# Optimization experiments

Measured on AMD Instinct MI355X. Metric: run time of the kernel, lower is better.

Reference implementation:

```python
import jax, jax.numpy as jnp
import numpy as np

N_NODES = 50000   # number of graph nodes
N_EDGES = 800000  # avg degree 16
D = 128           # in_dim == all hdims -> residual active every layer
L = 3             # len(cfg['hdims'])


def setup_inputs() -> dict:
    key = jax.random.key(0)
    ks = jax.random.split(key, 8)
    scale = 1.0 / np.sqrt(D)
    x = jax.random.normal(ks[0], (N_NODES, D), dtype=jnp.float32)
    edge_index = jax.random.randint(ks[1], (2, N_EDGES), 0, N_NODES, dtype=jnp.int32)
    in_fc_w = jax.random.normal(ks[2], (D, D), dtype=jnp.float32) * scale
    in_fc_b = jnp.zeros((D,), dtype=jnp.float32)
    # GraphConv per layer: lin_rel (with bias) applied to aggregated neighbors,
    # lin_root (no bias) applied to self features. All layers are DxD -> stack.
    w_rel = jax.random.normal(ks[3], (L, D, D), dtype=jnp.float32) * scale
    b_rel = jnp.zeros((L, D), dtype=jnp.float32)
    w_root = jax.random.normal(ks[4], (L, D, D), dtype=jnp.float32) * scale
    return {"x": x, "edge_index": edge_index, "in_fc_w": in_fc_w,
            "in_fc_b": in_fc_b, "w_rel": w_rel, "b_rel": b_rel, "w_root": w_root}


def reference(x, edge_index, in_fc_w, in_fc_b, w_rel, b_rel, w_root):
    src, dst = edge_index[0], edge_index[1]
    h = x @ in_fc_w + in_fc_b                     # in_fc
    for l in range(L):                            # fixed small layer count
        # GraphConv, aggr='add': gather source feats, scatter-add to targets
        agg = jax.ops.segment_sum(h[src], dst, num_segments=N_NODES)  # [N, D]
        out = agg @ w_rel[l] + b_rel[l] + h @ w_root[l]
        out = jax.nn.relu(out)
        h = out + h                               # residual (dims match)
    return h
```

## Files before the change

### kernel.cpp

```cpp
#include <hip/hip_runtime.h>
#include <hip/hip_bf16.h>


constexpr int D = 128;
constexpr int NB_SHIFT = 7;
constexpr int BCAP = 2560;
constexpr int CHUNK = 2048;

typedef __attribute__((ext_vector_type(8))) short bf16x8;
typedef __attribute__((ext_vector_type(4))) float f32x4;
typedef __attribute__((ext_vector_type(4))) unsigned int u32x4;

__device__ inline unsigned short f2bf(float f) {
    unsigned int u = __builtin_bit_cast(unsigned int, f);
    u += 0x7FFFu + ((u >> 16) & 1u);
    return (unsigned short)(u >> 16);
}
__device__ inline float bf2f(unsigned short v) {
    return __builtin_bit_cast(float, (unsigned int)v << 16);
}
__device__ inline float bf2f_lo(unsigned int v) {
    return __builtin_bit_cast(float, v << 16);
}
__device__ inline float bf2f_hi(unsigned int v) {
    return __builtin_bit_cast(float, v & 0xFFFF0000u);
}

__global__ __launch_bounds__(256) void prep(
    const float* __restrict__ x, const float* __restrict__ fc_w,
    const float* __restrict__ w_rel, const float* __restrict__ w_root,
    unsigned short* __restrict__ xb, unsigned short* __restrict__ Wp,
    int* __restrict__ cursor, int n4, int NB)
{
    int blk = blockIdx.x;
    const int nconv = (n4 + 255) / 256;
    if (blk < nconv) {
        int i = blk * 256 + threadIdx.x;
        if (i < n4) {
            float4 v = ((const float4*)x)[i];
            ushort4 o;
            o.x = f2bf(v.x); o.y = f2bf(v.y); o.z = f2bf(v.z); o.w = f2bf(v.w);
            ((ushort4*)xb)[i] = o;
        }
        return;
    }
    blk -= nconv;
    if (blk < 56) {
        int idx = blk * 256 + threadIdx.x;
        int mat  = idx >> 11;
        int rem  = idx & 2047;
        int tn   = rem >> 8;
        int ks   = (rem >> 6) & 3;
        int lane = rem & 63;
        const float* w = (mat == 0) ? fc_w
                       : (mat <= 3) ? w_rel  + (size_t)(mat - 1) * D * D
                                    : w_root + (size_t)(mat - 4) * D * D;
        unsigned short* wp = Wp + (size_t)mat * D * D + (size_t)rem * 8;
        int kbase = ks * 32 + (lane >> 4) * 8;
        int col   = tn * 16 + (lane & 15);
        #pragma unroll
        for (int j = 0; j < 8; ++j)
            wp[j] = f2bf(w[(size_t)(kbase + j) * D + col]);
        return;
    }
    blk -= 56;
    int i = blk * 256 + threadIdx.x;
    if (i < NB) cursor[i] = 0;
}

__global__ __launch_bounds__(256) void gemm_mfma(
    const unsigned short* __restrict__ A1, const unsigned short* __restrict__ W1p,
    const float* __restrict__ bias, unsigned short* __restrict__ hb_out, int N)
{
    const int tid  = threadIdx.x;
    const int wave = tid >> 6;
    const int lane = tid & 63;
    const int row0 = blockIdx.x * 64 + wave * 16;
    const int mrow = lane & 15;
    const int kgrp = lane >> 4;

    f32x4 acc[8];
    #pragma unroll
    for (int t = 0; t < 8; ++t) acc[t] = (f32x4){0.f, 0.f, 0.f, 0.f};

    int arow = row0 + mrow; if (arow >= N) arow = N - 1;
    const size_t abase = (size_t)arow * D + kgrp * 8;

    #pragma unroll
    for (int ks = 0; ks < 4; ++ks) {
        bf16x8 a1 = *(const bf16x8*)(A1 + abase + ks * 32);
        #pragma unroll
        for (int tn = 0; tn < 8; ++tn) {
            bf16x8 b = *(const bf16x8*)(W1p + ((size_t)((tn * 4 + ks) * 64 + lane) * 8));
            acc[tn] = __builtin_amdgcn_mfma_f32_16x16x32_bf16(a1, b, acc[tn], 0, 0, 0);
        }
    }

    const int r0 = row0 + kgrp * 4;
    #pragma unroll
    for (int tn = 0; tn < 8; ++tn) {
        const int col = tn * 16 + mrow;
        const float bv = bias[col];
        #pragma unroll
        for (int reg = 0; reg < 4; ++reg) {
            int r = r0 + reg;
            if (r < N) hb_out[(size_t)r * D + col] = f2bf(acc[tn][reg] + bv);
        }
    }
}

__global__ __launch_bounds__(256) void layer_fused(
    const unsigned short* __restrict__ hb_in, const int* __restrict__ rs4,
    const unsigned short* __restrict__ sorted_src,
    const unsigned short* __restrict__ Wrel, const unsigned short* __restrict__ Wroot,
    const float* __restrict__ bias,
    unsigned short* hb_out, float* out_f32, int N)
{
    __shared__ unsigned short aggt[16][136];

    const int tid   = threadIdx.x;
    const int wave  = tid >> 6;
    const int lane  = tid & 63;
    const int node0 = blockIdx.x * 16;

    {
        const int g = lane >> 4;
        const int c = lane & 15;
        const int n = node0 + wave * 4 + g;

        float acc[8];
        #pragma unroll
        for (int q = 0; q < 8; ++q) acc[q] = 0.f;

        if (n < N) {
            const int b = rs4[n << 2];
            const int e = rs4[(n << 2) + 4];
            int j = b;
            for (; j + 8 <= e; j += 8) {
                int s0 = sorted_src[j];
                int s1 = sorted_src[j + 1];
                int s2 = sorted_src[j + 2];
                int s3 = sorted_src[j + 3];
                int s4 = sorted_src[j + 4];
                int s5 = sorted_src[j + 5];
                int s6 = sorted_src[j + 6];
                int s7 = sorted_src[j + 7];
                u32x4 v0 = *(const u32x4*)((const unsigned int*)(hb_in + (size_t)s0 * D) + c * 4);
                u32x4 v1 = *(const u32x4*)((const unsigned int*)(hb_in + (size_t)s1 * D) + c * 4);
                u32x4 v2 = *(const u32x4*)((const unsigned int*)(hb_in + (size_t)s2 * D) + c * 4);
                u32x4 v3 = *(const u32x4*)((const unsigned int*)(hb_in + (size_t)s3 * D) + c * 4);
                u32x4 v4 = *(const u32x4*)((const unsigned int*)(hb_in + (size_t)s4 * D) + c * 4);
                u32x4 v5 = *(const u32x4*)((const unsigned int*)(hb_in + (size_t)s5 * D) + c * 4);
                u32x4 v6 = *(const u32x4*)((const unsigned int*)(hb_in + (size_t)s6 * D) + c * 4);
                u32x4 v7 = *(const u32x4*)((const unsigned int*)(hb_in + (size_t)s7 * D) + c * 4);
                #pragma unroll
                for (int q = 0; q < 4; ++q) {
                    acc[2 * q]     += ((bf2f_lo(v0[q]) + bf2f_lo(v1[q])) + (bf2f_lo(v2[q]) + bf2f_lo(v3[q])))
                                    + ((bf2f_lo(v4[q]) + bf2f_lo(v5[q])) + (bf2f_lo(v6[q]) + bf2f_lo(v7[q])));
                    acc[2 * q + 1] += ((bf2f_hi(v0[q]) + bf2f_hi(v1[q])) + (bf2f_hi(v2[q]) + bf2f_hi(v3[q])))
                                    + ((bf2f_hi(v4[q]) + bf2f_hi(v5[q])) + (bf2f_hi(v6[q]) + bf2f_hi(v7[q])));
                }
            }
            for (; j + 4 <= e; j += 4) {
                int s0 = sorted_src[j];
                int s1 = sorted_src[j + 1];
                int s2 = sorted_src[j + 2];
                int s3 = sorted_src[j + 3];
                u32x4 v0 = *(const u32x4*)((const unsigned int*)(hb_in + (size_t)s0 * D) + c * 4);
                u32x4 v1 = *(const u32x4*)((const unsigned int*)(hb_in + (size_t)s1 * D) + c * 4);
                u32x4 v2 = *(const u32x4*)((const unsigned int*)(hb_in + (size_t)s2 * D) + c * 4);
                u32x4 v3 = *(const u32x4*)((const unsigned int*)(hb_in + (size_t)s3 * D) + c * 4);
                #pragma unroll
                for (int q = 0; q < 4; ++q) {
                    acc[2 * q]     += (bf2f_lo(v0[q]) + bf2f_lo(v1[q])) + (bf2f_lo(v2[q]) + bf2f_lo(v3[q]));
                    acc[2 * q + 1] += (bf2f_hi(v0[q]) + bf2f_hi(v1[q])) + (bf2f_hi(v2[q]) + bf2f_hi(v3[q]));
                }
            }
            for (; j < e; ++j) {
                int s = sorted_src[j];
                u32x4 v = *(const u32x4*)((const unsigned int*)(hb_in + (size_t)s * D) + c * 4);
                #pragma unroll
                for (int q = 0; q < 4; ++q) {
                    acc[2 * q]     += bf2f_lo(v[q]);
                    acc[2 * q + 1] += bf2f_hi(v[q]);
                }
            }
        }
        u32x4 o;
        #pragma unroll
        for (int q = 0; q < 4; ++q)
            o[q] = (unsigned int)f2bf(acc[2 * q]) |
                   ((unsigned int)f2bf(acc[2 * q + 1]) << 16);
        *(u32x4*)&aggt[wave * 4 + g][c * 8] = o;
    }
    __syncthreads();

    const int mrow = lane & 15;
    const int kgrp = lane >> 4;

    f32x4 acc2[2];
    acc2[0] = (f32x4){0.f, 0.f, 0.f, 0.f};
    acc2[1] = (f32x4){0.f, 0.f, 0.f, 0.f};

    int arow = node0 + mrow; if (arow >= N) arow = N - 1;
    const size_t abase = (size_t)arow * D + kgrp * 8;

    #pragma unroll
    for (int ks = 0; ks < 4; ++ks) {
        bf16x8 a1 = *(const bf16x8*)&aggt[mrow][ks * 32 + kgrp * 8];
        bf16x8 a2 = *(const bf16x8*)(hb_in + abase + ks * 32);
        #pragma unroll
        for (int t = 0; t < 2; ++t) {
            const int tn = wave * 2 + t;
            bf16x8 b1 = *(const bf16x8*)(Wrel  + ((size_t)((tn * 4 + ks) * 64 + lane) * 8));
            acc2[t] = __builtin_amdgcn_mfma_f32_16x16x32_bf16(a1, b1, acc2[t], 0, 0, 0);
            bf16x8 b2 = *(const bf16x8*)(Wroot + ((size_t)((tn * 4 + ks) * 64 + lane) * 8));
            acc2[t] = __builtin_amdgcn_mfma_f32_16x16x32_bf16(a2, b2, acc2[t], 0, 0, 0);
        }
    }

    const int r0 = node0 + kgrp * 4;
    #pragma unroll
    for (int t = 0; t < 2; ++t) {
        const int tn  = wave * 2 + t;
        const int col = tn * 16 + mrow;
        const float bv = bias[col];
        #pragma unroll
        for (int reg = 0; reg < 4; ++reg) {
            int r = r0 + reg;
            if (r < N) {
                float z = fmaxf(acc2[t][reg] + bv, 0.f);
                float o = z + bf2f(hb_in[(size_t)r * D + col]);
                if (out_f32 != nullptr) out_f32[(size_t)r * D + col] = o;
                else                    hb_out[(size_t)r * D + col] = f2bf(o);
            }
        }
    }
}

__global__ __launch_bounds__(256) void bucket_scatter(
    const int* __restrict__ src, const int* __restrict__ dst,
    unsigned int* __restrict__ entries, int* __restrict__ cursor, int E, int NB)
{
    __shared__ unsigned int   stage[CHUNK];
    __shared__ unsigned short bslot[CHUNK];
    __shared__ int lhist[512];
    __shared__ int lscan[512];
    __shared__ int lgbase[512];
    __shared__ int lcur[512];
    __shared__ int sh[256];

    const int base  = blockIdx.x * CHUNK;
    const int count = min(CHUNK, E - base);
    const int tid   = threadIdx.x;

    for (int i = tid; i < 512; i += 256) { lhist[i] = 0; lcur[i] = 0; }
    __syncthreads();

    for (int i = tid; i < count; i += 256)
        atomicAdd(&lhist[dst[base + i] >> NB_SHIFT], 1);
    __syncthreads();

    int v2 = lhist[2 * tid] + lhist[2 * tid + 1];
    sh[tid] = v2;
    __syncthreads();
    #pragma unroll
    for (int off = 1; off < 256; off <<= 1) {
        int t = (tid >= off) ? sh[tid - off] : 0;
        __syncthreads();
        sh[tid] += t;
        __syncthreads();
    }
    int excl2 = sh[tid] - v2;
    lscan[2 * tid]     = excl2;
    lscan[2 * tid + 1] = excl2 + lhist[2 * tid];
    __syncthreads();

    for (int t = tid; t < 512; t += 256) {
        int c = (t < NB) ? lhist[t] : 0;
        lgbase[t] = (c > 0) ? atomicAdd(&cursor[t], c) : 0;
    }
    __syncthreads();

    for (int i = tid; i < count; i += 256) {
        int d = dst[base + i];
        int s = src[base + i];
        int b = d >> NB_SHIFT;
        int p = atomicAdd(&lcur[b], 1);
        int slot = lscan[b] + p;
        stage[slot] = ((unsigned int)(d & ((1 << NB_SHIFT) - 1)) << 16) | (unsigned int)s;
        bslot[slot] = (unsigned short)b;
    }
    __syncthreads();

    for (int i = tid; i < count; i += 256) {
        int b   = bslot[i];
        int off = i - lscan[b] + lgbase[b];
        if (off < BCAP) entries[(size_t)b * BCAP + off] = stage[i];
    }
}

__global__ __launch_bounds__(256) void bucket_sort(
    const unsigned int* __restrict__ entries, const int* __restrict__ cursor,
    unsigned short* __restrict__ sorted_src, int* __restrict__ rs4,
    int N, int NB, float inv_range)
{
    const int b   = blockIdx.x;
    const int tid = threadIdx.x;

    __shared__ int nhist[512];
    __shared__ int nscan[512];
    __shared__ int ncur[512];
    __shared__ int sh[256];
    __shared__ unsigned short svals[BCAP];
    __shared__ int sgbase;

    int part = 0;
    for (int i = tid; i < b; i += 256) part += min(cursor[i], BCAP);
    sh[tid] = part;
    __syncthreads();
    for (int off = 128; off > 0; off >>= 1) {
        if (tid < off) sh[tid] += sh[tid + off];
        __syncthreads();
    }
    if (tid == 0) sgbase = sh[0];
    const int cnt = min(cursor[b], BCAP);
    __syncthreads();
    const int gbase = sgbase;

    for (int i = tid; i < 512; i += 256) { nhist[i] = 0; ncur[i] = 0; }
    __syncthreads();

    const unsigned int* ebase = entries + (size_t)b * BCAP;
    for (int i = tid; i < cnt; i += 256) {
        unsigned int e = ebase[i];
        int s = (int)(e & 0xFFFFu);
        int r = (int)((float)s * inv_range); if (r > 3) r = 3;
        atomicAdd(&nhist[(int)((e >> 16) << 2) | r], 1);
    }
    __syncthreads();

    int v2 = nhist[2 * tid] + nhist[2 * tid + 1];
    sh[tid] = v2;
    __syncthreads();
    #pragma unroll
    for (int off = 1; off < 256; off <<= 1) {
        int t = (tid >= off) ? sh[tid - off] : 0;
        __syncthreads();
        sh[tid] += t;
        __syncthreads();
    }
    int excl2 = sh[tid] - v2;
    nscan[2 * tid]     = excl2;
    nscan[2 * tid + 1] = excl2 + nhist[2 * tid];
    __syncthreads();

    for (int i = tid; i < 512; i += 256) {
        int n = (b << NB_SHIFT) + (i >> 2);
        if (n < N) rs4[(n << 2) + (i & 3)] = gbase + nscan[i];
    }
    if (b == NB - 1 && tid == 0) rs4[N << 2] = gbase + cnt;

    for (int i = tid; i < cnt; i += 256) {
        unsigned int e = ebase[i];
        int s = (int)(e & 0xFFFFu);
        int r = (int)((float)s * inv_range); if (r > 3) r = 3;
        int key = (int)((e >> 16) << 2) | r;
        int p = atomicAdd(&ncur[key], 1);
        svals[nscan[key] + p] = (unsigned short)s;
    }
    __syncthreads();

    unsigned short* obase = sorted_src + gbase;
    for (int i = tid; i < cnt; i += 256) obase[i] = svals[i];
}

extern "C" void kernel_launch(void* const* d_in, const int* in_sizes, int n_in,
                              void* d_out, int out_size, void* d_ws, size_t ws_size,
                              hipStream_t stream)
{
    const float* x      = (const float*)d_in[0];
    const int*   ei     = (const int*)  d_in[1];
    const float* fc_w   = (const float*)d_in[2];
    const float* fc_b   = (const float*)d_in[3];
    const float* w_rel  = (const float*)d_in[4];
    const float* b_rel  = (const float*)d_in[5];
    const float* w_root = (const float*)d_in[6];
    float* out = (float*)d_out;

    const int N = in_sizes[0] / D;
    const int E = in_sizes[1] / 2;
    const int* src = ei;
    const int* dst = ei + E;
    const int NB = (N + (1 << NB_SHIFT) - 1) >> NB_SHIFT;

    char* p = (char*)d_ws;
    unsigned short* hb0  = (unsigned short*)p;  p += (size_t)N * D * sizeof(unsigned short);
    unsigned short* hb1  = (unsigned short*)p;  p += (size_t)N * D * sizeof(unsigned short);
    unsigned short* Wp   = (unsigned short*)p;  p += (size_t)7 * D * D * sizeof(unsigned short);
    unsigned int* entries = (unsigned int*)p;   p += (size_t)NB * BCAP * sizeof(unsigned int);
    unsigned short* sorted_src = (unsigned short*)p;  p += (size_t)E * sizeof(unsigned short);
    int* rs4    = (int*)p;                      p += (size_t)(4 * N + 4) * sizeof(int);
    int* cursor = (int*)p;                      p += (size_t)NB * sizeof(int);

    unsigned short* Wp_in   = Wp;
    unsigned short* Wp_rel  = Wp + (size_t)1 * D * D;
    unsigned short* Wp_root = Wp + (size_t)4 * D * D;
    unsigned short* xb = hb1;

    const int n4 = N * D / 4;
    const int gemm_blocks  = (N + 63) / 64;
    const int layer_blocks = (N + 15) / 16;
    const int prep_blocks  = (n4 + 255) / 256 + 56 + (NB + 255) / 256;

    prep<<<prep_blocks, 256, 0, stream>>>(x, fc_w, w_rel, w_root, xb, Wp, cursor, n4, NB);

    bucket_scatter<<<(E + CHUNK - 1) / CHUNK, 256, 0, stream>>>(
        src, dst, entries, cursor, E, NB);
    bucket_sort<<<NB, 256, 0, stream>>>(
        entries, cursor, sorted_src, rs4, N, NB, 4.0f / (float)N);

    gemm_mfma<<<gemm_blocks, 256, 0, stream>>>(xb, Wp_in, fc_b, hb0, N);

    unsigned short* hin  = hb0;
    unsigned short* hout = hb1;
    for (int l = 0; l < 3; ++l) {
        layer_fused<<<layer_blocks, 256, 0, stream>>>(
            hin, rs4, sorted_src,
            Wp_rel + (size_t)l * D * D, Wp_root + (size_t)l * D * D,
            b_rel + (size_t)l * D,
            (l == 2) ? nullptr : hout,
            (l == 2) ? out : nullptr, N);
        unsigned short* t = hin; hin = hout; hout = t;
    }
}
```

Before: 261.1 us.

## Pad per-node edge lists to multiples of eight with byte offsets

Bucket sort now writes each node's neighbor list as 32-bit byte offsets into the feature array, padded to a multiple of eight with entries that point to an appended all-zero row. The gather loop loads indices as vectors, prefetches the next group of eight, and drops the 4-wide and scalar tail loops. The global prefix sum over bucket counts is replaced by a fixed per-bucket stride, and the entries scratch buffer is placed in the output buffer. In exchange, index storage grows, padding adds wasted loads of the zero row, and a bucket whose padded total exceeds the stride would overflow.

```diff
diff --git a/kernel.cpp b/kernel.cpp
--- a/kernel.cpp
+++ b/kernel.cpp
@@ -5,6 +5,7 @@
 constexpr int D = 128;
 constexpr int NB_SHIFT = 7;
 constexpr int BCAP = 2560;
+constexpr int STRIDE = 3456;
 constexpr int CHUNK = 2048;
 
 typedef __attribute__((ext_vector_type(8))) short bf16x8;
@@ -30,7 +31,8 @@
     const float* __restrict__ x, const float* __restrict__ fc_w,
     const float* __restrict__ w_rel, const float* __restrict__ w_root,
     unsigned short* __restrict__ xb, unsigned short* __restrict__ Wp,
-    int* __restrict__ cursor, int n4, int NB)
+    int* __restrict__ cursor, unsigned short* __restrict__ hb0,
+    unsigned short* __restrict__ hb1, int n4, int NB, int N)
 {
     int blk = blockIdx.x;
     const int nconv = (n4 + 255) / 256;
@@ -64,8 +66,16 @@
         return;
     }
     blk -= 56;
-    int i = blk * 256 + threadIdx.x;
-    if (i < NB) cursor[i] = 0;
+    const int ncb = (NB + 255) / 256;
+    if (blk < ncb) {
+        int i = blk * 256 + threadIdx.x;
+        if (i < NB) cursor[i] = 0;
+        return;
+    }
+    if (threadIdx.x < 64)
+        ((unsigned int*)(hb0 + (size_t)N * D))[threadIdx.x] = 0u;
+    else if (threadIdx.x < 128)
+        ((unsigned int*)(hb1 + (size_t)N * D))[threadIdx.x - 64] = 0u;
 }
 
 __global__ __launch_bounds__(256) void gemm_mfma(
@@ -110,8 +120,8 @@
 }
 
 __global__ __launch_bounds__(256) void layer_fused(
-    const unsigned short* __restrict__ hb_in, const int* __restrict__ rs4,
-    const unsigned short* __restrict__ sorted_src,
+    const unsigned short* __restrict__ hb_in, const int* __restrict__ eb,
+    const unsigned int* __restrict__ sorted_off,
     const unsigned short* __restrict__ Wrel, const unsigned short* __restrict__ Wroot,
     const float* __restrict__ bias,
     unsigned short* hb_out, float* out_f32, int N)
@@ -133,56 +143,38 @@
         for (int q = 0; q < 8; ++q) acc[q] = 0.f;
 
         if (n < N) {
-            const int b = rs4[n << 2];
-            const int e = rs4[(n << 2) + 4];
-            int j = b;
-            for (; j + 8 <= e; j += 8) {
-                int s0 = sorted_src[j];
-                int s1 = sorted_src[j + 1];
-                int s2 = sorted_src[j + 2];
-                int s3 = sorted_src[j + 3];
-                int s4 = sorted_src[j + 4];
-                int s5 = sorted_src[j + 5];
-                int s6 = sorted_src[j + 6];
-                int s7 = sorted_src[j + 7];
-                u32x4 v0 = *(const u32x4*)((const unsigned int*)(hb_in + (size_t)s0 * D) + c * 4);
-                u32x4 v1 = *(const u32x4*)((const unsigned int*)(hb_in + (size_t)s1 * D) + c * 4);
-                u32x4 v2 = *(const u32x4*)((const unsigned int*)(hb_in + (size_t)s2 * D) + c * 4);
-                u32x4 v3 = *(const u32x4*)((const unsigned int*)(hb_in + (size_t)s3 * D) + c * 4);
-                u32x4 v4 = *(const u32x4*)((const unsigned int*)(hb_in + (size_t)s4 * D) + c * 4);
-                u32x4 v5 = *(const u32x4*)((const unsigned int*)(hb_in + (size_t)s5 * D) + c * 4);
-                u32x4 v6 = *(const u32x4*)((const unsigned int*)(hb_in + (size_t)s6 * D) + c * 4);
-                u32x4 v7 = *(const u32x4*)((const unsigned int*)(hb_in + (size_t)s7 * D) + c * 4);
-                #pragma unroll
-                for (int q = 0; q < 4; ++q) {
-                    acc[2 * q]     += ((bf2f_lo(v0[q]) + bf2f_lo(v1[q])) + (bf2f_lo(v2[q]) + bf2f_lo(v3[q])))
-                                    + ((bf2f_lo(v4[q]) + bf2f_lo(v5[q])) + (bf2f_lo(v6[q]) + bf2f_lo(v7[q])));
-                    acc[2 * q + 1] += ((bf2f_hi(v0[q]) + bf2f_hi(v1[q])) + (bf2f_hi(v2[q]) + bf2f_hi(v3[q])))
-                                    + ((bf2f_hi(v4[q]) + bf2f_hi(v5[q])) + (bf2f_hi(v6[q]) + bf2f_hi(v7[q])));
-                }
-            }
-            for (; j + 4 <= e; j += 4) {
-                int s0 = sorted_src[j];
-                int s1 = sorted_src[j + 1];
-                int s2 = sorted_src[j + 2];
-                int s3 = sorted_src[j + 3];
-                u32x4 v0 = *(const u32x4*)((const unsigned int*)(hb_in + (size_t)s0 * D) + c * 4);
-                u32x4 v1 = *(const u32x4*)((const unsigned int*)(hb_in + (size_t)s1 * D) + c * 4);
-                u32x4 v2 = *(const u32x4*)((const unsigned int*)(hb_in + (size_t)s2 * D) + c * 4);
-                u32x4 v3 = *(const u32x4*)((const unsigned int*)(hb_in + (size_t)s3 * D) + c * 4);
-                #pragma unroll
-                for (int q = 0; q < 4; ++q) {
-                    acc[2 * q]     += (bf2f_lo(v0[q]) + bf2f_lo(v1[q])) + (bf2f_lo(v2[q]) + bf2f_lo(v3[q]));
-                    acc[2 * q + 1] += (bf2f_hi(v0[q]) + bf2f_hi(v1[q])) + (bf2f_hi(v2[q]) + bf2f_hi(v3[q]));
-                }
-            }
-            for (; j < e; ++j) {
-                int s = sorted_src[j];
-                u32x4 v = *(const u32x4*)((const unsigned int*)(hb_in + (size_t)s * D) + c * 4);
-                #pragma unroll
-                for (int q = 0; q < 4; ++q) {
-                    acc[2 * q]     += bf2f_lo(v[q]);
-                    acc[2 * q + 1] += bf2f_hi(v[q]);
+            const int2 be = ((const int2*)eb)[n];
+            int j = be.x;
+            const int e = be.y;
+            const unsigned int c16 = (unsigned int)c * 16u;
+            const char* hb = (const char*)hb_in;
+            if (j < e) {
+                u32x4 iA = *(const u32x4*)(sorted_off + j);
+                u32x4 iB = *(const u32x4*)(sorted_off + j + 4);
+                for (;;) {
+                    u32x4 v0 = *(const u32x4*)(hb + (iA[0] + c16));
+                    u32x4 v1 = *(const u32x4*)(hb + (iA[1] + c16));
+                    u32x4 v2 = *(const u32x4*)(hb + (iA[2] + c16));
+                    u32x4 v3 = *(const u32x4*)(hb + (iA[3] + c16));
+                    u32x4 v4 = *(const u32x4*)(hb + (iB[0] + c16));
+                    u32x4 v5 = *(const u32x4*)(hb + (iB[1] + c16));
+                    u32x4 v6 = *(const u32x4*)(hb + (iB[2] + c16));
+                    u32x4 v7 = *(const u32x4*)(hb + (iB[3] + c16));
+                    const bool more = (j + 8 < e);
+                    u32x4 nA, nB;
+                    if (more) {
+                        nA = *(const u32x4*)(sorted_off + j + 8);
+                        nB = *(const u32x4*)(sorted_off + j + 12);
+                    }
+                    #pragma unroll
+                    for (int q = 0; q < 4; ++q) {
+                        acc[2 * q]     += ((bf2f_lo(v0[q]) + bf2f_lo(v1[q])) + (bf2f_lo(v2[q]) + bf2f_lo(v3[q])))
+                                        + ((bf2f_lo(v4[q]) + bf2f_lo(v5[q])) + (bf2f_lo(v6[q]) + bf2f_lo(v7[q])));
+                        acc[2 * q + 1] += ((bf2f_hi(v0[q]) + bf2f_hi(v1[q])) + (bf2f_hi(v2[q]) + bf2f_hi(v3[q])))
+                                        + ((bf2f_hi(v4[q]) + bf2f_hi(v5[q])) + (bf2f_hi(v6[q]) + bf2f_hi(v7[q])));
+                    }
+                    if (!more) break;
+                    iA = nA; iB = nB; j += 8;
                 }
             }
         }
@@ -302,8 +294,8 @@
 
 __global__ __launch_bounds__(256) void bucket_sort(
     const unsigned int* __restrict__ entries, const int* __restrict__ cursor,
-    unsigned short* __restrict__ sorted_src, int* __restrict__ rs4,
-    int N, int NB, float inv_range)
+    unsigned int* __restrict__ sorted_off, int* __restrict__ eb,
+    int N, int NB, float inv_range, unsigned int zero_off)
 {
     const int b   = blockIdx.x;
     const int tid = threadIdx.x;
@@ -311,22 +303,11 @@
     __shared__ int nhist[512];
     __shared__ int nscan[512];
     __shared__ int ncur[512];
+    __shared__ int nbase[129];
     __shared__ int sh[256];
-    __shared__ unsigned short svals[BCAP];
-    __shared__ int sgbase;
-
-    int part = 0;
-    for (int i = tid; i < b; i += 256) part += min(cursor[i], BCAP);
-    sh[tid] = part;
-    __syncthreads();
-    for (int off = 128; off > 0; off >>= 1) {
-        if (tid < off) sh[tid] += sh[tid + off];
-        __syncthreads();
-    }
-    if (tid == 0) sgbase = sh[0];
+    __shared__ unsigned int svals[STRIDE];
+
     const int cnt = min(cursor[b], BCAP);
-    __syncthreads();
-    const int gbase = sgbase;
 
     for (int i = tid; i < 512; i += 256) { nhist[i] = 0; ncur[i] = 0; }
     __syncthreads();
@@ -340,26 +321,40 @@
     }
     __syncthreads();
 
-    int v2 = nhist[2 * tid] + nhist[2 * tid + 1];
-    sh[tid] = v2;
-    __syncthreads();
-    #pragma unroll
-    for (int off = 1; off < 256; off <<= 1) {
-        int t = (tid >= off) ? sh[tid - off] : 0;
+    int c4 = 0, pc = 0;
+    if (tid < 128) {
+        c4 = nhist[4 * tid] + nhist[4 * tid + 1] + nhist[4 * tid + 2] + nhist[4 * tid + 3];
+        pc = (c4 + 7) & ~7;
+    }
+    sh[tid] = (tid < 128) ? pc : 0;
+    __syncthreads();
+    #pragma unroll
+    for (int off = 1; off < 128; off <<= 1) {
+        int t = (tid >= off && tid < 128) ? sh[tid - off] : 0;
         __syncthreads();
-        sh[tid] += t;
+        if (tid < 128) sh[tid] += t;
         __syncthreads();
     }
-    int excl2 = sh[tid] - v2;
-    nscan[2 * tid]     = excl2;
-    nscan[2 * tid + 1] = excl2 + nhist[2 * tid];
-    __syncthreads();
-
-    for (int i = tid; i < 512; i += 256) {
-        int n = (b << NB_SHIFT) + (i >> 2);
-        if (n < N) rs4[(n << 2) + (i & 3)] = gbase + nscan[i];
-    }
-    if (b == NB - 1 && tid == 0) rs4[N << 2] = gbase + cnt;
+    if (tid < 128) nbase[tid] = sh[tid] - pc;
+    if (tid == 127) nbase[128] = sh[127];
+    __syncthreads();
+    const int padded_total = nbase[128];
+
+    if (tid < 128) {
+        int base = nbase[tid];
+        int a0 = nhist[4 * tid], a1 = nhist[4 * tid + 1], a2 = nhist[4 * tid + 2];
+        nscan[4 * tid]     = base;
+        nscan[4 * tid + 1] = base + a0;
+        nscan[4 * tid + 2] = base + a0 + a1;
+        nscan[4 * tid + 3] = base + a0 + a1 + a2;
+        int nn = (b << NB_SHIFT) + tid;
+        if (nn < N) {
+            eb[2 * nn]     = b * STRIDE + base;
+            eb[2 * nn + 1] = b * STRIDE + base + pc;
+        }
+    }
+    for (int i = tid; i < padded_total; i += 256) svals[i] = zero_off;
+    __syncthreads();
 
     for (int i = tid; i < cnt; i += 256) {
         unsigned int e = ebase[i];
@@ -367,12 +362,12 @@
         int r = (int)((float)s * inv_range); if (r > 3) r = 3;
         int key = (int)((e >> 16) << 2) | r;
         int p = atomicAdd(&ncur[key], 1);
-        svals[nscan[key] + p] = (unsigned short)s;
-    }
-    __syncthreads();
-
-    unsigned short* obase = sorted_src + gbase;
-    for (int i = tid; i < cnt; i += 256) obase[i] = svals[i];
+        svals[nscan[key] + p] = ((unsigned int)s) << 8;
+    }
+    __syncthreads();
+
+    unsigned int* obase = sorted_off + (size_t)b * STRIDE;
+    for (int i = tid; i < padded_total; i += 256) obase[i] = svals[i];
 }
 
 extern "C" void kernel_launch(void* const* d_in, const int* in_sizes, int n_in,
@@ -395,13 +390,13 @@
     const int NB = (N + (1 << NB_SHIFT) - 1) >> NB_SHIFT;
 
     char* p = (char*)d_ws;
-    unsigned short* hb0  = (unsigned short*)p;  p += (size_t)N * D * sizeof(unsigned short);
-    unsigned short* hb1  = (unsigned short*)p;  p += (size_t)N * D * sizeof(unsigned short);
-    unsigned short* Wp   = (unsigned short*)p;  p += (size_t)7 * D * D * sizeof(unsigned short);
-    unsigned int* entries = (unsigned int*)p;   p += (size_t)NB * BCAP * sizeof(unsigned int);
-    unsigned short* sorted_src = (unsigned short*)p;  p += (size_t)E * sizeof(unsigned short);
-    int* rs4    = (int*)p;                      p += (size_t)(4 * N + 4) * sizeof(int);
-    int* cursor = (int*)p;                      p += (size_t)NB * sizeof(int);
+    unsigned short* hb0 = (unsigned short*)p;  p += (size_t)(N + 1) * D * sizeof(unsigned short);
+    unsigned short* hb1 = (unsigned short*)p;  p += (size_t)(N + 1) * D * sizeof(unsigned short);
+    unsigned short* Wp  = (unsigned short*)p;  p += (size_t)7 * D * D * sizeof(unsigned short);
+    unsigned int* sorted_off = (unsigned int*)p;  p += (size_t)NB * STRIDE * sizeof(unsigned int);
+    int* eb     = (int*)p;                     p += (size_t)2 * N * sizeof(int);
+    int* cursor = (int*)p;                     p += (size_t)NB * sizeof(int);
+    unsigned int* entries = (unsigned int*)d_out;
 
     unsigned short* Wp_in   = Wp;
     unsigned short* Wp_rel  = Wp + (size_t)1 * D * D;
@@ -411,14 +406,16 @@
     const int n4 = N * D / 4;
     const int gemm_blocks  = (N + 63) / 64;
     const int layer_blocks = (N + 15) / 16;
-    const int prep_blocks  = (n4 + 255) / 256 + 56 + (NB + 255) / 256;
-
-    prep<<<prep_blocks, 256, 0, stream>>>(x, fc_w, w_rel, w_root, xb, Wp, cursor, n4, NB);
+    const int prep_blocks  = (n4 + 255) / 256 + 56 + (NB + 255) / 256 + 1;
+
+    prep<<<prep_blocks, 256, 0, stream>>>(x, fc_w, w_rel, w_root, xb, Wp, cursor,
+                                          hb0, hb1, n4, NB, N);
 
     bucket_scatter<<<(E + CHUNK - 1) / CHUNK, 256, 0, stream>>>(
         src, dst, entries, cursor, E, NB);
     bucket_sort<<<NB, 256, 0, stream>>>(
-        entries, cursor, sorted_src, rs4, N, NB, 4.0f / (float)N);
+        entries, cursor, sorted_off, eb, N, NB, 4.0f / (float)N,
+        ((unsigned int)N) << 8);
 
     gemm_mfma<<<gemm_blocks, 256, 0, stream>>>(xb, Wp_in, fc_b, hb0, N);
 
@@ -426,7 +423,7 @@
     unsigned short* hout = hb1;
     for (int l = 0; l < 3; ++l) {
         layer_fused<<<layer_blocks, 256, 0, stream>>>(
-            hin, rs4, sorted_src,
+            hin, eb, sorted_off,
             Wp_rel + (size_t)l * D * D, Wp_root + (size_t)l * D * D,
             b_rel + (size_t)l * D,
             (l == 2) ? nullptr : hout,
```

Measured after the change: 239.2 us. 1.09x faster.
